# Optimization experiments

Measured on AMD Instinct MI355X. Metric: run time of the kernel, lower is better.

The kernel has to match this reference:

```python
import jax, jax.numpy as jnp
import numpy as np

N_NODES = 50000
N_EDGES = 800000
N_RELS = 65
D = 64
N_GRAPHS = 512


def setup_inputs() -> dict:
    key = jax.random.key(0)
    ks = jax.random.split(key, 20)
    inp = {
        "node_feats": jax.random.normal(ks[0], (N_NODES, D), dtype=jnp.float32),
        "etypes": jax.random.randint(ks[1], (N_EDGES,), 0, N_RELS),
        "src": jax.random.randint(ks[2], (N_EDGES,), 0, N_NODES),
        "dst": jax.random.randint(ks[3], (N_EDGES,), 0, N_NODES),
        "graph_ids": jnp.sort(jax.random.randint(ks[4], (N_NODES,), 0, N_GRAPHS)),
    }
    s = 1.0 / np.sqrt(D)
    # 3 RGCN layers: per-relation weights (basis with num_bases=num_rels == full) + bias
    for i, k in zip(range(1, 4), (ks[5], ks[6], ks[7])):
        inp[f"W_rel{i}"] = jax.random.normal(k, (N_RELS, D, D), dtype=jnp.float32) * s
        inp[f"b{i}"] = jnp.zeros((D,), dtype=jnp.float32)
    # 3 FC layers
    for i, k in zip(range(1, 4), (ks[8], ks[9], ks[10])):
        inp[f"fc_W{i}"] = jax.random.normal(k, (D, D), dtype=jnp.float32) * s
        inp[f"fc_b{i}"] = jnp.zeros((D,), dtype=jnp.float32)
    inp["pred_W"] = jax.random.normal(ks[11], (D, 2), dtype=jnp.float32) * s
    inp["pred_b"] = jnp.zeros((2,), dtype=jnp.float32)
    return inp


def _rgcn_layer(h, W, b, etypes, src, dst):
    # all-relation projection: [N, R, K]
    proj = jnp.einsum('nd,rdk->nrk', h, W)
    # per-edge gather of relation-specific message: [E, K]
    msg = proj[src, etypes]
    # scatter-sum into destination nodes
    agg = jax.ops.segment_sum(msg, dst, num_segments=h.shape[0])
    return jax.nn.relu(agg + b)


def reference(node_feats, etypes, src, dst, graph_ids,
              W_rel1, b1, W_rel2, b2, W_rel3, b3,
              fc_W1, fc_b1, fc_W2, fc_b2, fc_W3, fc_b3,
              pred_W, pred_b):
    h = node_feats
    h = _rgcn_layer(h, W_rel1, b1, etypes, src, dst)
    h = _rgcn_layer(h, W_rel2, b2, etypes, src, dst)
    h = _rgcn_layer(h, W_rel3, b3, etypes, src, dst)
    # sum-pool nodes per graph: [G, D]
    g = jax.ops.segment_sum(h, graph_ids, num_segments=N_GRAPHS)
    g = jax.nn.relu(g @ fc_W1 + fc_b1)
    g = jax.nn.relu(g @ fc_W2 + fc_b2)
    g = jax.nn.relu(g @ fc_W3 + fc_b3)
    return g @ pred_W + pred_b
```

## Files before the change

kernel.cpp:

```cpp
#include <hip/hip_runtime.h>
#include <hip/hip_bf16.h>

#define N_NODES 50000
#define N_EDGES 800000
#define N_RELS 65
#define DIM 64
#define N_GRAPHS 512

#define SORT_BLOCKS 2048
#define CHUNK ((N_EDGES + SORT_BLOCKS - 1) / SORT_BLOCKS)

#define SCAN_BLK 512
#define NSCAN_BLKS ((N_NODES + SCAN_BLK - 1) / SCAN_BLK)

#define MSG_BLOCKS 2048
#define NWAVES (MSG_BLOCKS * 4)

typedef __attribute__((ext_vector_type(8))) short short8;
typedef __attribute__((ext_vector_type(4))) float f32x4;


__global__ void conv_h_zero_kernel(const float* __restrict__ x, __hip_bfloat16* __restrict__ y,
                                   int* __restrict__ cnt_d, int* __restrict__ cnt_g) {
    int i = blockIdx.x * 256 + threadIdx.x;
    if (i < (N_NODES * DIM) / 4) {
        float4 v = *(const float4*)(x + (size_t)i * 4);
        unsigned short us[4];
        us[0] = __hip_bfloat16_raw(__float2bfloat16(v.x)).x;
        us[1] = __hip_bfloat16_raw(__float2bfloat16(v.y)).x;
        us[2] = __hip_bfloat16_raw(__float2bfloat16(v.z)).x;
        us[3] = __hip_bfloat16_raw(__float2bfloat16(v.w)).x;
        *(ushort4*)(y + (size_t)i * 4) = *(const ushort4*)us;
    }
    if (i < N_NODES) cnt_d[i] = 0;
    if (i < N_GRAPHS) cnt_g[i] = 0;
}


__global__ __launch_bounds__(256) void wconv_kernel(
    const float* __restrict__ W1, const float* __restrict__ W2,
    const float* __restrict__ W3,
    __hip_bfloat16* __restrict__ Wt1, __hip_bfloat16* __restrict__ Wt2,
    __hip_bfloat16* __restrict__ Wt3) {
    __shared__ float tile[64][65];
    int b = blockIdx.x;
    int which = b / N_RELS, r = b - which * N_RELS;
    const float* W = (which == 0) ? W1 : (which == 1) ? W2 : W3;
    __hip_bfloat16* Wt = (which == 0) ? Wt1 : (which == 1) ? Wt2 : Wt3;
    int t = threadIdx.x;
    for (int i = t; i < 4096; i += 256) {
        int row = i >> 6, col = i & 63;
        tile[row][col] = W[(size_t)r * 4096 + i];
    }
    __syncthreads();
    for (int i = t; i < 4096; i += 256) {
        int row = i >> 6, col = i & 63;
        Wt[(size_t)r * 4096 + i] = __float2bfloat16(tile[col][row]);
    }
}


__global__ __launch_bounds__(256) void hist_all_kernel(
    const int* __restrict__ et, const int* __restrict__ gid,
    int* __restrict__ blk_hist, int* __restrict__ cnt_g) {
    __shared__ int lh[N_RELS];
    int t = threadIdx.x, b = blockIdx.x;
    int gtid = b * 256 + t;
    if (t < N_RELS) lh[t] = 0;
    __syncthreads();
    int lo = b * CHUNK;
    int hi = lo + CHUNK; if (hi > N_EDGES) hi = N_EDGES;
    for (int i = lo + t; i < hi; i += 256)
        atomicAdd(&lh[et[i]], 1);
    for (int i = gtid; i < N_NODES; i += SORT_BLOCKS * 256)
        atomicAdd(&cnt_g[gid[i]], 1);
    __syncthreads();
    if (t < N_RELS) blk_hist[t * SORT_BLOCKS + b] = lh[t];
}


__global__ __launch_bounds__(1024) void relwave2_kernel(const int* __restrict__ blk_hist,
                                                        int* __restrict__ blk_off,
                                                        int* __restrict__ rel_ptr,
                                                        int* __restrict__ tile_base) {
    __shared__ int tot[N_RELS];
    int t = threadIdx.x;
    int w = t >> 6, lane = t & 63;
    for (int r = w; r < N_RELS; r += 16) {
        int run = 0;
        for (int c = 0; c < SORT_BLOCKS; c += 64) {
            int b = c + lane;
            int v = blk_hist[r * SORT_BLOCKS + b];
            int x = v;
            #pragma unroll
            for (int off = 1; off < 64; off <<= 1) {
                int y = __shfl_up(x, off);
                if (lane >= off) x += y;
            }
            blk_off[r * SORT_BLOCKS + b] = run + x - v;
            run += __shfl(x, 63);
        }
        if (lane == 0) tot[r] = run;
    }
    __syncthreads();
    if (t == 0) {
        int s = 0, tt = 0;
        for (int q = 0; q < N_RELS; ++q) {
            rel_ptr[q] = s; s += tot[q];
            tile_base[q] = tt; tt += (tot[q] + 15) >> 4;
        }
        rel_ptr[N_RELS] = N_EDGES;
        tile_base[N_RELS] = tt;
    }
}


__global__ __launch_bounds__(256) void scatter2_kernel(
    const int* __restrict__ et, const int* __restrict__ src,
    const int* __restrict__ dst, const int* __restrict__ blk_off,
    const int* __restrict__ rel_ptr,
    unsigned long long* __restrict__ epk, int* __restrict__ cnt_d) {
    __shared__ int cur[N_RELS];
    int t = threadIdx.x, b = blockIdx.x;
    if (t < N_RELS) cur[t] = blk_off[t * SORT_BLOCKS + b] + rel_ptr[t];
    __syncthreads();
    int lo = b * CHUNK;
    int hi = lo + CHUNK; if (hi > N_EDGES) hi = N_EDGES;

    bool val[4]; int rr[4], dd[4]; unsigned ss[4];
    #pragma unroll
    for (int k = 0; k < 4; ++k) {
        int i = lo + t + k * 256;
        val[k] = (i < hi);
        int ic = val[k] ? i : lo;
        rr[k] = et[ic]; dd[k] = dst[ic]; ss[k] = (unsigned)src[ic];
    }
    int p[4];
    #pragma unroll
    for (int k = 0; k < 4; ++k)
        if (val[k]) p[k] = atomicAdd(&cur[rr[k]], 1);
    int rk[4];
    #pragma unroll
    for (int k = 0; k < 4; ++k)
        if (val[k]) rk[k] = atomicAdd(&cnt_d[dd[k]], 1);
    #pragma unroll
    for (int k = 0; k < 4; ++k)
        if (val[k]) {
            unsigned lo32 = ss[k] | ((unsigned)dd[k] << 16);
            epk[p[k]] = (unsigned long long)lo32 |
                        ((unsigned long long)(unsigned)rk[k] << 32);
        }
}


__global__ __launch_bounds__(SCAN_BLK) void scanblk_kernel(const int* __restrict__ cnt,
                                                           int* __restrict__ outv,
                                                           int* __restrict__ blk_tot) {
    __shared__ int tmp[SCAN_BLK];
    int t = threadIdx.x;
    int i = blockIdx.x * SCAN_BLK + t;
    int v = (i < N_NODES) ? cnt[i] : 0;
    tmp[t] = v;
    __syncthreads();
    for (int off = 1; off < SCAN_BLK; off <<= 1) {
        int add = (t >= off) ? tmp[t - off] : 0;
        __syncthreads();
        tmp[t] += add;
        __syncthreads();
    }
    if (i < N_NODES) outv[i] = tmp[t] - v;
    if (t == SCAN_BLK - 1) blk_tot[blockIdx.x] = tmp[t];
}

__global__ __launch_bounds__(64) void scantop_gid_kernel(
    const int* __restrict__ blk_tot, int* __restrict__ blk_base,
    const int* __restrict__ cnt_g, int* __restrict__ g_ptr) {
    int lane = threadIdx.x;
    if (blockIdx.x == 0) {
        if (lane == 0) {
            int run = 0;
            for (int b = 0; b < NSCAN_BLKS; ++b) { blk_base[b] = run; run += blk_tot[b]; }
        }
    } else {
        int run = 0;
        for (int c = 0; c < N_GRAPHS; c += 64) {
            int v = cnt_g[c + lane];
            int x = v;
            #pragma unroll
            for (int off = 1; off < 64; off <<= 1) {
                int y = __shfl_up(x, off);
                if (lane >= off) x += y;
            }
            g_ptr[c + lane] = run + x - v;
            run += __shfl(x, 63);
        }
    }
}

__global__ __launch_bounds__(SCAN_BLK) void scanadd_kernel(int* __restrict__ outv,
                                                           const int* __restrict__ blk_base) {
    int i = blockIdx.x * SCAN_BLK + threadIdx.x;
    if (i < N_NODES) outv[i] += blk_base[blockIdx.x];
}

__global__ void unpack_kernel(const unsigned long long* __restrict__ epk,
                              const int* __restrict__ row_ptr,
                              int* __restrict__ src_s, int* __restrict__ dpos) {
    int i = blockIdx.x * 256 + threadIdx.x;
    if (i < N_EDGES) {
        unsigned long long e = epk[i];
        int s = (int)(e & 0xFFFFu);
        int d = (int)((e >> 16) & 0xFFFFu);
        int rank = (int)(e >> 32);
        src_s[i] = s;
        dpos[i] = rank + row_ptr[d];
    }
}


__device__ inline unsigned pack2bf(float x, float y) {
    unsigned short ux = __hip_bfloat16_raw(__float2bfloat16(x)).x;
    unsigned short uy = __hip_bfloat16_raw(__float2bfloat16(y)).x;
    return (unsigned)ux | ((unsigned)uy << 16);
}

__global__ __launch_bounds__(256) void msg_mfma_kernel(
    const __hip_bfloat16* __restrict__ hb, const __hip_bfloat16* __restrict__ Wt,
    const int* __restrict__ rel_ptr, const int* __restrict__ tile_base,
    const int* __restrict__ src_s, const int* __restrict__ dpos,
    __hip_bfloat16* __restrict__ msg) {
    int t = threadIdx.x;
    int w = t >> 6, lane = t & 63;
    int quad = lane >> 4, m16 = lane & 15;
    int wave = blockIdx.x * 4 + w;

    int ntiles = tile_base[N_RELS];
    int tpw = (ntiles + NWAVES - 1) / NWAVES;
    int T = wave * tpw;
    int T1 = T + tpw; if (T1 > ntiles) T1 = ntiles;
    if (T >= T1) return;

    int r = 0;
    while (T >= tile_base[r + 1]) ++r;

    while (T < T1) {
        int chunk_end = tile_base[r + 1]; if (chunk_end > T1) chunk_end = T1;
        int e_base = rel_ptr[r], t_base = tile_base[r];
        int seg_end = rel_ptr[r + 1];

        const __hip_bfloat16* Wr = Wt + (size_t)r * (DIM * DIM);
        short8 bf00 = *(const short8*)(Wr + (2 * m16)      * DIM + quad * 8);
        short8 bf01 = *(const short8*)(Wr + (2 * m16 + 1)  * DIM + quad * 8);
        short8 bf02 = *(const short8*)(Wr + (32 + 2 * m16) * DIM + quad * 8);
        short8 bf03 = *(const short8*)(Wr + (33 + 2 * m16) * DIM + quad * 8);
        short8 bf10 = *(const short8*)(Wr + (2 * m16)      * DIM + 32 + quad * 8);
        short8 bf11 = *(const short8*)(Wr + (2 * m16 + 1)  * DIM + 32 + quad * 8);
        short8 bf12 = *(const short8*)(Wr + (32 + 2 * m16) * DIM + 32 + quad * 8);
        short8 bf13 = *(const short8*)(Wr + (33 + 2 * m16) * DIM + 32 + quad * 8);

        auto loadidx = [&](int TT, int& sv, int& dp) {
            int TC = TT < chunk_end ? TT : chunk_end - 1;
            int i = e_base + (TC - t_base) * 16 + lane;
            if (i >= N_EDGES) i = N_EDGES - 1;
            sv = src_s[i]; dp = dpos[i];
        };
        auto gatherA = [&](int sv, short8& x0, short8& x1) {
            int s = __shfl(sv, m16);
            const __hip_bfloat16* hp = hb + (size_t)s * DIM + quad * 8;
            x0 = *(const short8*)hp;
            x1 = *(const short8*)(hp + 32);
        };

        int sv0, dp0, sv1, dp1, sv2, dp2;
        short8 a0c, a1c, a0n, a1n;
        loadidx(T,     sv0, dp0);
        loadidx(T + 1, sv1, dp1);
        gatherA(sv0, a0c, a1c);

        for (; T < chunk_end; ++T) {
            loadidx(T + 2, sv2, dp2);
            gatherA(sv1, a0n, a1n);

            int e0 = e_base + (T - t_base) * 16;
            int rows = seg_end - e0; if (rows > 16) rows = 16;

            f32x4 c0 = {0.f, 0.f, 0.f, 0.f}, c1 = c0, c2 = c0, c3 = c0;
            c0 = __builtin_amdgcn_mfma_f32_16x16x32_bf16(a0c, bf00, c0, 0, 0, 0);
            c1 = __builtin_amdgcn_mfma_f32_16x16x32_bf16(a0c, bf01, c1, 0, 0, 0);
            c2 = __builtin_amdgcn_mfma_f32_16x16x32_bf16(a0c, bf02, c2, 0, 0, 0);
            c3 = __builtin_amdgcn_mfma_f32_16x16x32_bf16(a0c, bf03, c3, 0, 0, 0);
            c0 = __builtin_amdgcn_mfma_f32_16x16x32_bf16(a1c, bf10, c0, 0, 0, 0);
            c1 = __builtin_amdgcn_mfma_f32_16x16x32_bf16(a1c, bf11, c1, 0, 0, 0);
            c2 = __builtin_amdgcn_mfma_f32_16x16x32_bf16(a1c, bf12, c2, 0, 0, 0);
            c3 = __builtin_amdgcn_mfma_f32_16x16x32_bf16(a1c, bf13, c3, 0, 0, 0);

            int dpr[4];
            #pragma unroll
            for (int g = 0; g < 4; ++g) dpr[g] = __shfl(dp0, quad * 4 + g);

            #pragma unroll
            for (int g = 0; g < 4; ++g) {
                if (quad * 4 + g < rows) {
                    unsigned plo = pack2bf(c0[g], c1[g]);
                    unsigned phi = pack2bf(c2[g], c3[g]);
                    __hip_bfloat16* mp = msg + (size_t)dpr[g] * DIM;
                    *(unsigned*)(mp + 2 * m16) = plo;
                    *(unsigned*)(mp + 32 + 2 * m16) = phi;
                }
            }

            sv0 = sv1; dp0 = dp1; sv1 = sv2; dp1 = dp2;
            a0c = a0n; a1c = a1n;
        }
        ++r;
        while (T < T1 && T >= tile_base[r + 1]) ++r;
    }
}


__global__ __launch_bounds__(256) void agg_kernel(
    const __hip_bfloat16* __restrict__ msg, const int* __restrict__ row_ptr,
    const int* __restrict__ cnt_d, const float* __restrict__ b,
    __hip_bfloat16* __restrict__ hout) {
    int wave = blockIdx.x * 4 + (threadIdx.x >> 6);
    int lane = threadIdx.x & 63;
    if (wave >= N_NODES) return;
    int j0 = row_ptr[wave];
    int n  = cnt_d[wave];
    int rgrp = lane >> 3, dgrp = lane & 7;

    float a[8] = {0.f, 0.f, 0.f, 0.f, 0.f, 0.f, 0.f, 0.f};
    for (int jj = 0; jj < n; jj += 8) {
        int row = jj + rgrp;
        if (row < n) {
            uint4 d = *(const uint4*)(msg + (size_t)(j0 + row) * DIM + dgrp * 8);
            a[0] += __uint_as_float(d.x << 16);
            a[1] += __uint_as_float(d.x & 0xffff0000u);
            a[2] += __uint_as_float(d.y << 16);
            a[3] += __uint_as_float(d.y & 0xffff0000u);
            a[4] += __uint_as_float(d.z << 16);
            a[5] += __uint_as_float(d.z & 0xffff0000u);
            a[6] += __uint_as_float(d.w << 16);
            a[7] += __uint_as_float(d.w & 0xffff0000u);
        }
    }
    #pragma unroll
    for (int i = 0; i < 8; ++i) {
        a[i] += __shfl_xor(a[i], 8);
        a[i] += __shfl_xor(a[i], 16);
        a[i] += __shfl_xor(a[i], 32);
    }
    if (rgrp == 0) {
        unsigned short us[8];
        #pragma unroll
        for (int i = 0; i < 8; ++i) {
            float v = a[i] + b[dgrp * 8 + i];
            us[i] = __hip_bfloat16_raw(__float2bfloat16(v > 0.f ? v : 0.f)).x;
        }
        *(uint4*)(hout + (size_t)wave * DIM + dgrp * 8) = *(const uint4*)us;
    }
}


__global__ __launch_bounds__(256) void poolfc_kernel(
    const __hip_bfloat16* __restrict__ h, const int* __restrict__ g_ptr,
    const int* __restrict__ cnt_g,
    const float* __restrict__ W1, const float* __restrict__ b1,
    const float* __restrict__ W2, const float* __restrict__ b2,
    const float* __restrict__ W3, const float* __restrict__ b3,
    const float* __restrict__ pW, const float* __restrict__ pb,
    float* __restrict__ out) {
    int wave = blockIdx.x * 4 + (threadIdx.x >> 6);
    int lane = threadIdx.x & 63;
    if (wave >= N_GRAPHS) return;
    int j0 = g_ptr[wave];
    int n  = cnt_g[wave];
    int rgrp = lane >> 3, dgrp = lane & 7;

    float a[8] = {0.f, 0.f, 0.f, 0.f, 0.f, 0.f, 0.f, 0.f};
    for (int jj = 0; jj < n; jj += 8) {
        int row = jj + rgrp;
        if (row < n) {
            uint4 d = *(const uint4*)(h + (size_t)(j0 + row) * DIM + dgrp * 8);
            a[0] += __uint_as_float(d.x << 16);
            a[1] += __uint_as_float(d.x & 0xffff0000u);
            a[2] += __uint_as_float(d.y << 16);
            a[3] += __uint_as_float(d.y & 0xffff0000u);
            a[4] += __uint_as_float(d.z << 16);
            a[5] += __uint_as_float(d.z & 0xffff0000u);
            a[6] += __uint_as_float(d.w << 16);
            a[7] += __uint_as_float(d.w & 0xffff0000u);
        }
    }
    #pragma unroll
    for (int i = 0; i < 8; ++i) {
        a[i] += __shfl_xor(a[i], 8);
        a[i] += __shfl_xor(a[i], 16);
        a[i] += __shfl_xor(a[i], 32);
    }
    float v;
    {
        float acc = b1[lane];
        #pragma unroll
        for (int o = 0; o < 8; ++o)
            #pragma unroll
            for (int q = 0; q < 8; ++q)
                acc += __shfl(a[o], q) * W1[(q * 8 + o) * DIM + lane];
        v = acc > 0.f ? acc : 0.f;
    }
    {
        float acc = b2[lane];
        #pragma unroll
        for (int d = 0; d < DIM; ++d)
            acc += __shfl(v, d) * W2[d * DIM + lane];
        v = acc > 0.f ? acc : 0.f;
    }
    {
        float acc = b3[lane];
        #pragma unroll
        for (int d = 0; d < DIM; ++d)
            acc += __shfl(v, d) * W3[d * DIM + lane];
        v = acc > 0.f ? acc : 0.f;
    }
    float p0 = v * pW[lane * 2 + 0];
    float p1 = v * pW[lane * 2 + 1];
    #pragma unroll
    for (int off = 32; off > 0; off >>= 1) {
        p0 += __shfl_down(p0, off);
        p1 += __shfl_down(p1, off);
    }
    if (lane == 0) {
        out[wave * 2 + 0] = p0 + pb[0];
        out[wave * 2 + 1] = p1 + pb[1];
    }
}


extern "C" void kernel_launch(void* const* d_in, const int* in_sizes, int n_in,
                              void* d_out, int out_size, void* d_ws, size_t ws_size,
                              hipStream_t stream) {
    const float* node_feats = (const float*)d_in[0];
    const int*   etypes     = (const int*)d_in[1];
    const int*   src        = (const int*)d_in[2];
    const int*   dst        = (const int*)d_in[3];
    const int*   graph_ids  = (const int*)d_in[4];
    const float* W1 = (const float*)d_in[5];
    const float* b1 = (const float*)d_in[6];
    const float* W2 = (const float*)d_in[7];
    const float* b2 = (const float*)d_in[8];
    const float* W3 = (const float*)d_in[9];
    const float* b3 = (const float*)d_in[10];
    const float* fcW1 = (const float*)d_in[11];
    const float* fcb1 = (const float*)d_in[12];
    const float* fcW2 = (const float*)d_in[13];
    const float* fcb2 = (const float*)d_in[14];
    const float* fcW3 = (const float*)d_in[15];
    const float* fcb3 = (const float*)d_in[16];
    const float* pW = (const float*)d_in[17];
    const float* pb = (const float*)d_in[18];
    float* out = (float*)d_out;

    char* p = (char*)d_ws;
    auto alloc = [&](size_t bytes) -> void* {
        void* r = (void*)p;
        p += (bytes + 255) & ~(size_t)255;
        return r;
    };
    int* blk_hist  = (int*)alloc((size_t)SORT_BLOCKS * N_RELS * sizeof(int));
    int* blk_off   = (int*)alloc((size_t)SORT_BLOCKS * N_RELS * sizeof(int));
    int* rel_ptr   = (int*)alloc((N_RELS + 1) * sizeof(int));
    int* tile_base = (int*)alloc((N_RELS + 1) * sizeof(int));
    unsigned long long* epk = (unsigned long long*)alloc((size_t)N_EDGES * sizeof(unsigned long long));
    int* src_s     = (int*)alloc((size_t)N_EDGES * sizeof(int));
    int* dpos      = (int*)alloc((size_t)N_EDGES * sizeof(int));
    int* cnt_d     = (int*)alloc((size_t)N_NODES * sizeof(int));
    int* row_ptr   = (int*)alloc((size_t)N_NODES * sizeof(int));
    int* blk_tot   = (int*)alloc(NSCAN_BLKS * sizeof(int));
    int* blk_base  = (int*)alloc(NSCAN_BLKS * sizeof(int));
    int* cnt_g     = (int*)alloc(N_GRAPHS * sizeof(int));
    int* g_ptr     = (int*)alloc(N_GRAPHS * sizeof(int));
    __hip_bfloat16* hb0 = (__hip_bfloat16*)alloc((size_t)N_NODES * DIM * sizeof(__hip_bfloat16));
    __hip_bfloat16* hb1 = (__hip_bfloat16*)alloc((size_t)N_NODES * DIM * sizeof(__hip_bfloat16));
    __hip_bfloat16* Wt1 = (__hip_bfloat16*)alloc((size_t)N_RELS * DIM * DIM * sizeof(__hip_bfloat16));
    __hip_bfloat16* Wt2 = (__hip_bfloat16*)alloc((size_t)N_RELS * DIM * DIM * sizeof(__hip_bfloat16));
    __hip_bfloat16* Wt3 = (__hip_bfloat16*)alloc((size_t)N_RELS * DIM * DIM * sizeof(__hip_bfloat16));
    __hip_bfloat16* msg = (__hip_bfloat16*)alloc((size_t)N_EDGES * DIM * sizeof(__hip_bfloat16));

    const int EBLK = (N_EDGES + 255) / 256;
    const int CBLK = (N_NODES * DIM / 4 + 255) / 256;
    const int AGG_BLOCKS = (N_NODES + 3) / 4;

    conv_h_zero_kernel<<<CBLK, 256, 0, stream>>>(node_feats, hb0, cnt_d, cnt_g);
    wconv_kernel<<<3 * N_RELS, 256, 0, stream>>>(W1, W2, W3, Wt1, Wt2, Wt3);
    hist_all_kernel<<<SORT_BLOCKS, 256, 0, stream>>>(etypes, graph_ids, blk_hist, cnt_g);
    relwave2_kernel<<<1, 1024, 0, stream>>>(blk_hist, blk_off, rel_ptr, tile_base);
    scatter2_kernel<<<SORT_BLOCKS, 256, 0, stream>>>(etypes, src, dst, blk_off, rel_ptr,
                                                     epk, cnt_d);
    scanblk_kernel<<<NSCAN_BLKS, SCAN_BLK, 0, stream>>>(cnt_d, row_ptr, blk_tot);
    scantop_gid_kernel<<<2, 64, 0, stream>>>(blk_tot, blk_base, cnt_g, g_ptr);
    scanadd_kernel<<<NSCAN_BLKS, SCAN_BLK, 0, stream>>>(row_ptr, blk_base);
    unpack_kernel<<<EBLK, 256, 0, stream>>>(epk, row_ptr, src_s, dpos);

    msg_mfma_kernel<<<MSG_BLOCKS, 256, 0, stream>>>(hb0, Wt1, rel_ptr, tile_base,
                                                    src_s, dpos, msg);
    agg_kernel<<<AGG_BLOCKS, 256, 0, stream>>>(msg, row_ptr, cnt_d, b1, hb1);

    msg_mfma_kernel<<<MSG_BLOCKS, 256, 0, stream>>>(hb1, Wt2, rel_ptr, tile_base,
                                                    src_s, dpos, msg);
    agg_kernel<<<AGG_BLOCKS, 256, 0, stream>>>(msg, row_ptr, cnt_d, b2, hb0);

    msg_mfma_kernel<<<MSG_BLOCKS, 256, 0, stream>>>(hb0, Wt3, rel_ptr, tile_base,
                                                    src_s, dpos, msg);
    agg_kernel<<<AGG_BLOCKS, 256, 0, stream>>>(msg, row_ptr, cnt_d, b3, hb1);

    poolfc_kernel<<<(N_GRAPHS + 3) / 4, 256, 0, stream>>>(hb1, g_ptr, cnt_g,
                                                          fcW1, fcb1, fcW2, fcb2,
                                                          fcW3, fcb3, pW, pb, out);
}
```

Measured before the change: 420.5 us.

## Parallelize relation offset scan across blocks and widen message stores

Replaces the single-block relation scan with one 256-thread block per relation that does vectorized loads, a per-thread serial sum, a wave scan and a cross-wave combine. A tiny follow-up kernel then builds rel_ptr and tile_base. This removes a serial bottleneck where 16 waves walked 2048 entries for each of 65 relations, at the cost of one extra launch. Separately, the MFMA message kernel now loads weight columns 4*m16..4*m16+3 so each lane can write 4 contiguous bf16 values with one 8-byte store instead of two 4-byte stores.

After: 385.5 us. 8.3% less time.

```diff
diff --git a/kernel.cpp b/kernel.cpp
--- a/kernel.cpp
+++ b/kernel.cpp
@@ -79,35 +79,49 @@
 }
 
 
-__global__ __launch_bounds__(1024) void relwave2_kernel(const int* __restrict__ blk_hist,
-                                                        int* __restrict__ blk_off,
-                                                        int* __restrict__ rel_ptr,
-                                                        int* __restrict__ tile_base) {
-    __shared__ int tot[N_RELS];
+__global__ __launch_bounds__(256) void relscan_kernel(const int* __restrict__ blk_hist,
+                                                      int* __restrict__ blk_off,
+                                                      int* __restrict__ rel_tot) {
+    __shared__ int wsum[4];
+    int r = blockIdx.x;
     int t = threadIdx.x;
     int w = t >> 6, lane = t & 63;
-    for (int r = w; r < N_RELS; r += 16) {
-        int run = 0;
-        for (int c = 0; c < SORT_BLOCKS; c += 64) {
-            int b = c + lane;
-            int v = blk_hist[r * SORT_BLOCKS + b];
-            int x = v;
-            #pragma unroll
-            for (int off = 1; off < 64; off <<= 1) {
-                int y = __shfl_up(x, off);
-                if (lane >= off) x += y;
-            }
-            blk_off[r * SORT_BLOCKS + b] = run + x - v;
-            run += __shfl(x, 63);
-        }
-        if (lane == 0) tot[r] = run;
-    }
+    const int PER = SORT_BLOCKS / 256;
+    int4 v0 = *(const int4*)(blk_hist + (size_t)r * SORT_BLOCKS + t * PER);
+    int4 v1 = *(const int4*)(blk_hist + (size_t)r * SORT_BLOCKS + t * PER + 4);
+    int vals[8] = {v0.x, v0.y, v0.z, v0.w, v1.x, v1.y, v1.z, v1.w};
+    int s = 0;
+    #pragma unroll
+    for (int j = 0; j < 8; ++j) s += vals[j];
+    int x = s;
+    #pragma unroll
+    for (int off = 1; off < 64; off <<= 1) {
+        int y = __shfl_up(x, off);
+        if (lane >= off) x += y;
+    }
+    if (lane == 63) wsum[w] = x;
     __syncthreads();
-    if (t == 0) {
+    int base = 0;
+    for (int i = 0; i < w; ++i) base += wsum[i];
+    int run = base + x - s;
+    int out[8];
+    #pragma unroll
+    for (int j = 0; j < 8; ++j) { out[j] = run; run += vals[j]; }
+    *(int4*)(blk_off + (size_t)r * SORT_BLOCKS + t * PER)     = *(const int4*)&out[0];
+    *(int4*)(blk_off + (size_t)r * SORT_BLOCKS + t * PER + 4) = *(const int4*)&out[4];
+    if (t == 255) rel_tot[r] = base + x;
+}
+
+
+__global__ __launch_bounds__(64) void reltop_kernel(const int* __restrict__ rel_tot,
+                                                    int* __restrict__ rel_ptr,
+                                                    int* __restrict__ tile_base) {
+    if (threadIdx.x == 0) {
         int s = 0, tt = 0;
         for (int q = 0; q < N_RELS; ++q) {
-            rel_ptr[q] = s; s += tot[q];
-            tile_base[q] = tt; tt += (tot[q] + 15) >> 4;
+            int v = rel_tot[q];
+            rel_ptr[q] = s; s += v;
+            tile_base[q] = tt; tt += (v + 15) >> 4;
         }
         rel_ptr[N_RELS] = N_EDGES;
         tile_base[N_RELS] = tt;
@@ -249,14 +263,14 @@
         int seg_end = rel_ptr[r + 1];
 
         const __hip_bfloat16* Wr = Wt + (size_t)r * (DIM * DIM);
-        short8 bf00 = *(const short8*)(Wr + (2 * m16)      * DIM + quad * 8);
-        short8 bf01 = *(const short8*)(Wr + (2 * m16 + 1)  * DIM + quad * 8);
-        short8 bf02 = *(const short8*)(Wr + (32 + 2 * m16) * DIM + quad * 8);
-        short8 bf03 = *(const short8*)(Wr + (33 + 2 * m16) * DIM + quad * 8);
-        short8 bf10 = *(const short8*)(Wr + (2 * m16)      * DIM + 32 + quad * 8);
-        short8 bf11 = *(const short8*)(Wr + (2 * m16 + 1)  * DIM + 32 + quad * 8);
-        short8 bf12 = *(const short8*)(Wr + (32 + 2 * m16) * DIM + 32 + quad * 8);
-        short8 bf13 = *(const short8*)(Wr + (33 + 2 * m16) * DIM + 32 + quad * 8);
+        short8 bf00 = *(const short8*)(Wr + (4 * m16)     * DIM + quad * 8);
+        short8 bf01 = *(const short8*)(Wr + (4 * m16 + 1) * DIM + quad * 8);
+        short8 bf02 = *(const short8*)(Wr + (4 * m16 + 2) * DIM + quad * 8);
+        short8 bf03 = *(const short8*)(Wr + (4 * m16 + 3) * DIM + quad * 8);
+        short8 bf10 = *(const short8*)(Wr + (4 * m16)     * DIM + 32 + quad * 8);
+        short8 bf11 = *(const short8*)(Wr + (4 * m16 + 1) * DIM + 32 + quad * 8);
+        short8 bf12 = *(const short8*)(Wr + (4 * m16 + 2) * DIM + 32 + quad * 8);
+        short8 bf13 = *(const short8*)(Wr + (4 * m16 + 3) * DIM + 32 + quad * 8);
 
         auto loadidx = [&](int TT, int& sv, int& dp) {
             int TC = TT < chunk_end ? TT : chunk_end - 1;
@@ -301,11 +315,10 @@
             #pragma unroll
             for (int g = 0; g < 4; ++g) {
                 if (quad * 4 + g < rows) {
-                    unsigned plo = pack2bf(c0[g], c1[g]);
-                    unsigned phi = pack2bf(c2[g], c3[g]);
-                    __hip_bfloat16* mp = msg + (size_t)dpr[g] * DIM;
-                    *(unsigned*)(mp + 2 * m16) = plo;
-                    *(unsigned*)(mp + 32 + 2 * m16) = phi;
+                    uint2 pk;
+                    pk.x = pack2bf(c0[g], c1[g]);
+                    pk.y = pack2bf(c2[g], c3[g]);
+                    *(uint2*)(msg + (size_t)dpr[g] * DIM + 4 * m16) = pk;
                 }
             }
 
@@ -469,6 +482,7 @@
     int* blk_hist  = (int*)alloc((size_t)SORT_BLOCKS * N_RELS * sizeof(int));
     int* blk_off   = (int*)alloc((size_t)SORT_BLOCKS * N_RELS * sizeof(int));
     int* rel_ptr   = (int*)alloc((N_RELS + 1) * sizeof(int));
+    int* rel_tot   = (int*)alloc(N_RELS * sizeof(int));
     int* tile_base = (int*)alloc((N_RELS + 1) * sizeof(int));
     unsigned long long* epk = (unsigned long long*)alloc((size_t)N_EDGES * sizeof(unsigned long long));
     int* src_s     = (int*)alloc((size_t)N_EDGES * sizeof(int));
@@ -493,7 +507,8 @@
     conv_h_zero_kernel<<<CBLK, 256, 0, stream>>>(node_feats, hb0, cnt_d, cnt_g);
     wconv_kernel<<<3 * N_RELS, 256, 0, stream>>>(W1, W2, W3, Wt1, Wt2, Wt3);
     hist_all_kernel<<<SORT_BLOCKS, 256, 0, stream>>>(etypes, graph_ids, blk_hist, cnt_g);
-    relwave2_kernel<<<1, 1024, 0, stream>>>(blk_hist, blk_off, rel_ptr, tile_base);
+    relscan_kernel<<<N_RELS, 256, 0, stream>>>(blk_hist, blk_off, rel_tot);
+    reltop_kernel<<<1, 64, 0, stream>>>(rel_tot, rel_ptr, tile_base);
     scatter2_kernel<<<SORT_BLOCKS, 256, 0, stream>>>(etypes, src, dst, blk_off, rel_ptr,
                                                      epk, cnt_d);
     scanblk_kernel<<<NSCAN_BLKS, SCAN_BLK, 0, stream>>>(cnt_d, row_ptr, blk_tot);
```
